# Kernel optimization log

Hardware: AMD Instinct MI355X
Metric: run time of the kernel (lower is better)

## Reference

```python
import jax, jax.numpy as jnp
import numpy as np
import math

B, T, E, H, DH, FH, L, V = 64, 256, 256, 8, 256, 1024, 6, 65
NEG = -1.0e9


def layer_norm(x, g, b, eps=1e-5):
    mu = jnp.mean(x, axis=-1, keepdims=True)
    var = jnp.var(x, axis=-1, keepdims=True)
    return (x - mu) / jnp.sqrt(var + eps) * g + b


def setup_inputs() -> dict:
    key = jax.random.key(0)
    ks = jax.random.split(key, 24)
    s = 0.02
    inp = {
        "tokens": jax.random.randint(ks[0], (B, T), 0, V, dtype=jnp.int32),
        "emb": jax.random.normal(ks[1], (V, E), jnp.float32) * s,
        # per-layer, per-head QKV weights stacked: [L, H, E, DH]
        "Wk": jax.random.normal(ks[2], (L, H, E, DH), jnp.float32) * s,
        "Wq": jax.random.normal(ks[3], (L, H, E, DH), jnp.float32) * s,
        "Wv": jax.random.normal(ks[4], (L, H, E, DH), jnp.float32) * s,
        "bk": jnp.zeros((L, H, DH), jnp.float32),
        "bq": jnp.zeros((L, H, DH), jnp.float32),
        "bv": jnp.zeros((L, H, DH), jnp.float32),
        "Wp": jax.random.normal(ks[5], (L, H * DH, E), jnp.float32) * s,
        "bp": jnp.zeros((L, E), jnp.float32),
        # one LayerNorm per block, reused twice (matches original module)
        "ln_g": jnp.ones((L, E), jnp.float32),
        "ln_b": jnp.zeros((L, E), jnp.float32),
        "W1": jax.random.normal(ks[6], (L, E, FH), jnp.float32) * s,
        "b1": jnp.zeros((L, FH), jnp.float32),
        "W2": jax.random.normal(ks[7], (L, FH, E), jnp.float32) * s,
        "b2": jnp.zeros((L, E), jnp.float32),
        "Wc1": jax.random.normal(ks[8], (E, FH), jnp.float32) * s,
        "bc1": jnp.zeros((FH,), jnp.float32),
        "Wc2": jax.random.normal(ks[9], (FH, V), jnp.float32) * s,
        "bc2": jnp.zeros((V,), jnp.float32),
    }
    return inp


def reference(tokens, emb, Wk, Wq, Wv, bk, bq, bv, Wp, bp, ln_g, ln_b,
              W1, b1, W2, b2, Wc1, bc1, Wc2, bc2):
    # embedding + (degenerate) positional encoding: pos table is all zeros,
    # so pos_encode reduces to x * sqrt(n_embd)
    x = emb[tokens] * math.sqrt(E)  # [B, T, E]
    # causal mask: positions where tril==0 (strict upper triangle) are masked
    mask = ~jnp.tril(jnp.ones((T, T), dtype=bool))  # True => masked
    scale = 1.0 / math.sqrt(DH)
    for i in range(L):
        K = jnp.einsum('bte,hed->bhtd', x, Wk[i]) + bk[i][None, :, None, :]
        Q = jnp.einsum('bte,hed->bhtd', x, Wq[i]) + bq[i][None, :, None, :]
        Vv = jnp.einsum('bte,hed->bhtd', x, Wv[i]) + bv[i][None, :, None, :]
        # NOTE: original computes Score = K @ Q^T (K and Q roles swapped)
        scores = jnp.einsum('bhtd,bhsd->bhts', K, Q) * scale
        scores = jnp.where(mask, NEG, scores)
        attn = jax.nn.softmax(scores, axis=-1)
        out = jnp.einsum('bhts,bhsd->bhtd', attn, Vv)  # [B,H,T,DH]
        out = out.transpose(0, 2, 1, 3).reshape(B, T, H * DH)
        proj = out @ Wp[i] + bp[i]
        mid = layer_norm(x + proj, ln_g[i], ln_b[i])
        ffn = jax.nn.relu(mid @ W1[i] + b1[i]) @ W2[i] + b2[i]
        x = layer_norm(mid + ffn, ln_g[i], ln_b[i])
    logits = jax.nn.relu(x @ Wc1 + bc1) @ Wc2 + bc2  # [B, T, V]
    return logits
```

## Files before the change

kernel.cpp:

```cpp
#include <hip/hip_runtime.h>
#include <hip/hip_bf16.h>

#define BB 64
#define TT 256
#define EE 256
#define HH 8
#define DHD 256
#define FFH 1024
#define LL 6
#define VV 65
#define NCHK 4
#define CB (BB / NCHK)
#define CNT (CB * TT)

typedef float f32x4 __attribute__((ext_vector_type(4)));
typedef short bf16x8 __attribute__((ext_vector_type(8)));
typedef unsigned short u16x8 __attribute__((ext_vector_type(8)));
typedef unsigned short u16x4 __attribute__((ext_vector_type(4)));

__device__ __forceinline__ unsigned short f2b(float f) {
  union { float f; unsigned u; } x; x.f = f;
  unsigned r = x.u + 0x7fffu + ((x.u >> 16) & 1u);
  return (unsigned short)(r >> 16);
}

#define BMT 128
#define BNT 128
#define BKT 32
#define LSTR 40

struct GP2 {
  const unsigned short* A; int lda; long sA;
  const unsigned short* B; int ldb; long sB;
  void* C; int ldc;
  int divC; long sC0, sC1;
  int rsplit; long sRowOuter;
  const float* bias; long sBias;
  const float* resid; int ldr;
  int N, K;
  float scale;
};

template<int OUTMODE, bool HAS_BIAS, bool RELU, bool HAS_RESID, bool MASKED,
         bool CAUSALK, bool NCHECK>
__global__ __launch_bounds__(256) void mfma_gemm(GP2 p) {
  __shared__ unsigned short As[BMT * LSTR];
  __shared__ unsigned short Bs[BNT * LSTR];
  const int tid  = threadIdx.x;
  const int m0   = blockIdx.x * BMT;
  const int n0   = blockIdx.y * BNT;
  const int z    = blockIdx.z;
  const int lane = tid & 63;
  const int wid  = tid >> 6;
  const int wm   = (wid >> 1) * 64, wn = (wid & 1) * 64;
  const int lr   = lane & 15;
  const int kq   = lane >> 4;

  const long zoff = (long)(z / p.divC) * p.sC0 + (long)(z % p.divC) * p.sC1;

  if constexpr (MASKED) {
    if (n0 >= m0 + BMT) {
      float* Cf = (float*)p.C;
#pragma unroll
      for (int fm = 0; fm < 4; ++fm)
#pragma unroll
        for (int r = 0; r < 4; ++r) {
          int m = m0 + wm + fm * 16 + kq * 4 + r;
          long ro = zoff + (long)(m / p.rsplit) * p.sRowOuter
                         + (long)(m % p.rsplit) * p.ldc;
#pragma unroll
          for (int fn = 0; fn < 4; ++fn) {
            int n = n0 + wn + fn * 16 + lr;
            Cf[ro + n] = -1.0e9f;
          }
        }
      return;
    }
  }

  const unsigned short* Az = p.A + (long)z * p.sA;
  const unsigned short* Bz = p.B + (long)z * p.sB;

  f32x4 acc[4][4] = {};

  const int kEnd = CAUSALK ? ((p.K < m0 + BMT) ? p.K : (m0 + BMT)) : p.K;
  for (int k0 = 0; k0 < kEnd; k0 += BKT) {
#pragma unroll
    for (int u0 = 0; u0 < 2; ++u0) {
      int u = tid + u0 * 256;
      int row = u >> 2, seg = (u & 3) << 3;
      u16x8 v = *(const u16x8*)(Az + (long)(m0 + row) * p.lda + (k0 + seg));
      *(u16x8*)&As[row * LSTR + seg] = v;
    }
#pragma unroll
    for (int u0 = 0; u0 < 2; ++u0) {
      int u = tid + u0 * 256;
      int row = u >> 2, seg = (u & 3) << 3;
      u16x8 v = {0, 0, 0, 0, 0, 0, 0, 0};
      if (!NCHECK || (n0 + row < p.N))
        v = *(const u16x8*)(Bz + (long)(n0 + row) * p.ldb + (k0 + seg));
      *(u16x8*)&Bs[row * LSTR + seg] = v;
    }
    __syncthreads();
    bf16x8 af[4], bv[4];
#pragma unroll
    for (int f = 0; f < 4; ++f) {
      af[f] = *(const bf16x8*)&As[(wm + f * 16 + lr) * LSTR + kq * 8];
      bv[f] = *(const bf16x8*)&Bs[(wn + f * 16 + lr) * LSTR + kq * 8];
    }
#pragma unroll
    for (int fm = 0; fm < 4; ++fm)
#pragma unroll
      for (int fn = 0; fn < 4; ++fn)
        acc[fm][fn] = __builtin_amdgcn_mfma_f32_16x16x32_bf16(
            af[fm], bv[fn], acc[fm][fn], 0, 0, 0);
    __syncthreads();
  }

  const float* bias = nullptr;
  if constexpr (HAS_BIAS) bias = p.bias + (long)z * p.sBias;

#pragma unroll
  for (int fm = 0; fm < 4; ++fm)
#pragma unroll
    for (int fn = 0; fn < 4; ++fn) {
      f32x4 a = acc[fm][fn];
      int n = n0 + wn + fn * 16 + lr;
      if constexpr (NCHECK) { if (n >= p.N) continue; }
      if constexpr (OUTMODE == 2) {
        int mb = m0 + wm + fm * 16 + kq * 4;
        long off = zoff + (long)(mb / p.rsplit) * p.sRowOuter
                        + (long)n * p.ldc + (mb % p.rsplit);
        u16x4 w;
#pragma unroll
        for (int r = 0; r < 4; ++r) {
          float v = a[r];
          if constexpr (HAS_BIAS) v += bias[n];
          w[r] = f2b(v);
        }
        *(u16x4*)((unsigned short*)p.C + off) = w;
      } else {
#pragma unroll
        for (int r = 0; r < 4; ++r) {
          int m = m0 + wm + fm * 16 + kq * 4 + r;
          long off = zoff + (long)(m / p.rsplit) * p.sRowOuter
                          + (long)(m % p.rsplit) * p.ldc + n;
          float v = a[r];
          if constexpr (HAS_BIAS) v += bias[n];
          if constexpr (MASKED) v = (n <= m) ? v * p.scale : -1.0e9f;
          if constexpr (HAS_RESID) v += p.resid[(long)m * p.ldr + n];
          if constexpr (RELU) v = fmaxf(v, 0.0f);
          if constexpr (OUTMODE == 0) ((float*)p.C)[off] = v;
          else ((unsigned short*)p.C)[off] = f2b(v);
        }
      }
    }
}

__global__ __launch_bounds__(256) void transpose_b_k(const float* __restrict__ in,
                                                     unsigned short* __restrict__ out,
                                                     int R, int C, long sIn, long sOut) {
  __shared__ float t[32][33];
  const int z = blockIdx.z;
  in += (long)z * sIn; out += (long)z * sOut;
  const int c0 = blockIdx.x * 32, r0 = blockIdx.y * 32;
  const int tx = threadIdx.x & 31, ty = threadIdx.x >> 5;
#pragma unroll
  for (int i = 0; i < 4; ++i) {
    int r = r0 + ty + i * 8;
    if (r < R && c0 + tx < C) t[ty + i * 8][tx] = in[(long)r * C + c0 + tx];
  }
  __syncthreads();
#pragma unroll
  for (int i = 0; i < 4; ++i) {
    int rr = r0 + tx, cc = c0 + ty + i * 8;
    if (rr < R && cc < C) out[(long)cc * R + rr] = f2b(t[tx][ty + i * 8]);
  }
}

__global__ __launch_bounds__(256) void softmax_k(const float* __restrict__ S,
                                                 unsigned short* __restrict__ P) {
  const int t = blockIdx.x;
  const long z = blockIdx.y;
  const float* row = S + z * (long)(TT * TT) + (long)t * TT;
  unsigned short* prow = P + z * (long)(TT * TT) + (long)t * TT;
  const int tid = threadIdx.x;
  float v = row[tid];
  float m = v;
#pragma unroll
  for (int off = 32; off; off >>= 1) m = fmaxf(m, __shfl_xor(m, off));
  __shared__ float red[8];
  if ((tid & 63) == 0) red[tid >> 6] = m;
  __syncthreads();
  m = fmaxf(fmaxf(red[0], red[1]), fmaxf(red[2], red[3]));
  float e = __expf(v - m);
  float s = e;
#pragma unroll
  for (int off = 32; off; off >>= 1) s += __shfl_xor(s, off);
  if ((tid & 63) == 0) red[4 + (tid >> 6)] = s;
  __syncthreads();
  s = red[4] + red[5] + red[6] + red[7];
  prow[tid] = f2b(e / s);
}

__global__ __launch_bounds__(256) void ln_k(float* __restrict__ x,
                                            unsigned short* __restrict__ xb,
                                            const float* __restrict__ g,
                                            const float* __restrict__ b) {
  const long row = blockIdx.x;
  const int tid = threadIdx.x;
  float* p = x + row * EE;
  float v = p[tid];
  float s = v, s2 = v * v;
#pragma unroll
  for (int off = 32; off; off >>= 1) {
    s += __shfl_xor(s, off);
    s2 += __shfl_xor(s2, off);
  }
  __shared__ float r1[4], r2[4];
  if ((tid & 63) == 0) { r1[tid >> 6] = s; r2[tid >> 6] = s2; }
  __syncthreads();
  s = r1[0] + r1[1] + r1[2] + r1[3];
  s2 = r2[0] + r2[1] + r2[2] + r2[3];
  float mu = s * (1.0f / EE);
  float var = fmaxf(s2 * (1.0f / EE) - mu * mu, 0.0f);
  float rn = rsqrtf(var + 1e-5f);
  float o = (v - mu) * rn * g[tid] + b[tid];
  p[tid] = o;
  xb[row * EE + tid] = f2b(o);
}

__global__ __launch_bounds__(256) void embed_k(const int* __restrict__ tok,
                                               const float* __restrict__ emb,
                                               float* __restrict__ X,
                                               unsigned short* __restrict__ Xb) {
  const long n = blockIdx.x;
  const int e = threadIdx.x;
  float v = emb[(long)tok[n] * EE + e] * 16.0f;
  X[n * EE + e] = v;
  Xb[n * EE + e] = f2b(v);
}

__global__ void tripwire_k(float* out, float code) { out[0] = code; }

extern "C" void kernel_launch(void* const* d_in, const int* in_sizes, int n_in,
                              void* d_out, int out_size, void* d_ws, size_t ws_size,
                              hipStream_t stream) {
  const int*   tokens = (const int*)d_in[0];
  const float* emb  = (const float*)d_in[1];
  const float* Wk   = (const float*)d_in[2];
  const float* Wq   = (const float*)d_in[3];
  const float* Wv   = (const float*)d_in[4];
  const float* bk   = (const float*)d_in[5];
  const float* bq   = (const float*)d_in[6];
  const float* bv   = (const float*)d_in[7];
  const float* Wp   = (const float*)d_in[8];
  const float* bp   = (const float*)d_in[9];
  const float* lng  = (const float*)d_in[10];
  const float* lnb  = (const float*)d_in[11];
  const float* W1   = (const float*)d_in[12];
  const float* b1   = (const float*)d_in[13];
  const float* W2   = (const float*)d_in[14];
  const float* b2   = (const float*)d_in[15];
  const float* Wc1  = (const float*)d_in[16];
  const float* bc1  = (const float*)d_in[17];
  const float* Wc2  = (const float*)d_in[18];
  const float* bc2  = (const float*)d_in[19];
  float* out = (float*)d_out;

  const long NT   = (long)BB * TT;
  const long CTD  = (long)CB * HH * TT * DHD;
  const long CTT  = (long)CB * HH * TT * TT;

  if (ws_size < 183109632UL) {
    tripwire_k<<<1, 1, 0, stream>>>(out, -100000.0f - (float)(ws_size >> 20));
    return;
  }

  char* w = (char*)d_ws;
  float* X   = (float*)w;            w += NT * EE * 4;
  float* MID = (float*)w;            w += NT * EE * 4;
  unsigned short* Xb   = (unsigned short*)w; w += NT * EE * 2;
  unsigned short* MIDb = (unsigned short*)w; w += NT * EE * 2;
  unsigned short* CK   = (unsigned short*)w; w += CTD * 2;
  unsigned short* CQ   = (unsigned short*)w; w += CTD * 2;
  unsigned short* CVt  = (unsigned short*)w; w += CTD * 2;
  float* CSb = (float*)w;            w += CTT * 4;
  unsigned short* CPb  = (unsigned short*)w; w += CTT * 2;
  unsigned short* Wkt  = (unsigned short*)w; w += (long)LL * HH * DHD * EE * 2;
  unsigned short* Wqt  = (unsigned short*)w; w += (long)LL * HH * DHD * EE * 2;
  unsigned short* Wvt  = (unsigned short*)w; w += (long)LL * HH * DHD * EE * 2;
  unsigned short* Wpt  = (unsigned short*)w; w += (long)LL * EE * (HH * DHD) * 2;
  unsigned short* W1t  = (unsigned short*)w; w += (long)LL * FFH * EE * 2;
  unsigned short* W2t  = (unsigned short*)w; w += (long)LL * EE * FFH * 2;
  unsigned short* Wc1t = (unsigned short*)w; w += (long)FFH * EE * 2;
  unsigned short* Wc2t = (unsigned short*)w; w += (long)VV * FFH * 2;
  unsigned short* AO = CK;
  unsigned short* H1 = (unsigned short*)CSb;

  transpose_b_k<<<dim3(8, 8, LL * HH), 256, 0, stream>>>(Wk, Wkt, EE, DHD, (long)EE * DHD, (long)DHD * EE);
  transpose_b_k<<<dim3(8, 8, LL * HH), 256, 0, stream>>>(Wq, Wqt, EE, DHD, (long)EE * DHD, (long)DHD * EE);
  transpose_b_k<<<dim3(8, 8, LL * HH), 256, 0, stream>>>(Wv, Wvt, EE, DHD, (long)EE * DHD, (long)DHD * EE);
  transpose_b_k<<<dim3(8, 64, LL), 256, 0, stream>>>(Wp, Wpt, HH * DHD, EE, (long)HH * DHD * EE, (long)EE * HH * DHD);
  transpose_b_k<<<dim3(32, 8, LL), 256, 0, stream>>>(W1, W1t, EE, FFH, (long)EE * FFH, (long)FFH * EE);
  transpose_b_k<<<dim3(8, 32, LL), 256, 0, stream>>>(W2, W2t, FFH, EE, (long)FFH * EE, (long)EE * FFH);
  transpose_b_k<<<dim3(32, 8, 1), 256, 0, stream>>>(Wc1, Wc1t, EE, FFH, 0, 0);
  transpose_b_k<<<dim3(3, 32, 1), 256, 0, stream>>>(Wc2, Wc2t, FFH, VV, 0, 0);

  embed_k<<<NT, 256, 0, stream>>>(tokens, emb, X, Xb);

  for (int i = 0; i < LL; ++i) {
    for (int c = 0; c < NCHK; ++c) {
      const long RB = (long)c * CNT;
      for (int m3 = 0; m3 < 3; ++m3) {
        GP2 p{};
        p.A = Xb + RB * EE; p.lda = EE; p.sA = 0;
        p.B = (m3 == 0 ? Wkt : m3 == 1 ? Wqt : Wvt) + (long)i * HH * DHD * EE;
        p.ldb = EE; p.sB = (long)DHD * EE;
        p.divC = 1; p.sC1 = 0;
        p.rsplit = TT;
        p.bias = (m3 == 0 ? bk : m3 == 1 ? bq : bv) + (long)i * HH * DHD;
        p.sBias = DHD;
        p.N = DHD; p.K = EE;
        if (m3 < 2) {
          p.C = (m3 == 0 ? CK : CQ); p.ldc = DHD;
          p.sC0 = (long)TT * DHD; p.sRowOuter = (long)HH * TT * DHD;
          mfma_gemm<1, true, false, false, false, false, false>
              <<<dim3(CNT / BMT, DHD / BNT, HH), 256, 0, stream>>>(p);
        } else {
          p.C = CVt; p.ldc = TT;
          p.sC0 = (long)DHD * TT; p.sRowOuter = (long)HH * DHD * TT;
          mfma_gemm<2, true, false, false, false, false, false>
              <<<dim3(CNT / BMT, DHD / BNT, HH), 256, 0, stream>>>(p);
        }
      }
      {
        GP2 p{};
        p.A = CK; p.lda = DHD; p.sA = (long)TT * DHD;
        p.B = CQ; p.ldb = DHD; p.sB = (long)TT * DHD;
        p.C = CSb; p.ldc = TT;
        p.divC = 1; p.sC0 = (long)TT * TT; p.sC1 = 0;
        p.rsplit = 1 << 30; p.sRowOuter = 0;
        p.N = TT; p.K = DHD; p.scale = 0.0625f;
        mfma_gemm<0, false, false, false, true, false, false>
            <<<dim3(TT / BMT, TT / BNT, CB * HH), 256, 0, stream>>>(p);
      }
      softmax_k<<<dim3(TT, CB * HH), 256, 0, stream>>>(CSb, CPb);
      {
        GP2 p{};
        p.A = CPb; p.lda = TT; p.sA = (long)TT * TT;
        p.B = CVt; p.ldb = TT; p.sB = (long)DHD * TT;
        p.C = AO; p.ldc = HH * DHD;
        p.divC = HH; p.sC0 = (long)TT * HH * DHD; p.sC1 = DHD;
        p.rsplit = 1 << 30; p.sRowOuter = 0;
        p.N = DHD; p.K = TT;
        mfma_gemm<1, false, false, false, false, true, false>
            <<<dim3(TT / BMT, DHD / BNT, CB * HH), 256, 0, stream>>>(p);
      }
      {
        GP2 p{};
        p.A = AO; p.lda = HH * DHD; p.sA = 0;
        p.B = Wpt + (long)i * EE * HH * DHD; p.ldb = HH * DHD; p.sB = 0;
        p.C = MID + RB * EE; p.ldc = EE;
        p.divC = 1; p.sC0 = 0; p.sC1 = 0; p.rsplit = 1 << 30; p.sRowOuter = 0;
        p.bias = bp + (long)i * EE; p.sBias = 0;
        p.resid = X + RB * EE; p.ldr = EE;
        p.N = EE; p.K = HH * DHD;
        mfma_gemm<0, true, false, true, false, false, false>
            <<<dim3(CNT / BMT, EE / BNT, 1), 256, 0, stream>>>(p);
      }
    }
    ln_k<<<NT, 256, 0, stream>>>(MID, MIDb, lng + (long)i * EE, lnb + (long)i * EE);
    {
      GP2 p{};
      p.A = MIDb; p.lda = EE; p.sA = 0;
      p.B = W1t + (long)i * FFH * EE; p.ldb = EE; p.sB = 0;
      p.C = H1; p.ldc = FFH;
      p.divC = 1; p.sC0 = 0; p.sC1 = 0; p.rsplit = 1 << 30; p.sRowOuter = 0;
      p.bias = b1 + (long)i * FFH; p.sBias = 0;
      p.N = FFH; p.K = EE;
      mfma_gemm<1, true, true, false, false, false, false>
          <<<dim3(NT / BMT, FFH / BNT, 1), 256, 0, stream>>>(p);
    }
    {
      GP2 p{};
      p.A = H1; p.lda = FFH; p.sA = 0;
      p.B = W2t + (long)i * EE * FFH; p.ldb = FFH; p.sB = 0;
      p.C = X; p.ldc = EE;
      p.divC = 1; p.sC0 = 0; p.sC1 = 0; p.rsplit = 1 << 30; p.sRowOuter = 0;
      p.bias = b2 + (long)i * EE; p.sBias = 0;
      p.resid = MID; p.ldr = EE;
      p.N = EE; p.K = FFH;
      mfma_gemm<0, true, false, true, false, false, false>
          <<<dim3(NT / BMT, EE / BNT, 1), 256, 0, stream>>>(p);
    }
    ln_k<<<NT, 256, 0, stream>>>(X, Xb, lng + (long)i * EE, lnb + (long)i * EE);
  }

  {
    GP2 p{};
    p.A = Xb; p.lda = EE; p.sA = 0;
    p.B = Wc1t; p.ldb = EE; p.sB = 0;
    p.C = H1; p.ldc = FFH;
    p.divC = 1; p.sC0 = 0; p.sC1 = 0; p.rsplit = 1 << 30; p.sRowOuter = 0;
    p.bias = bc1; p.sBias = 0;
    p.N = FFH; p.K = EE;
    mfma_gemm<1, true, true, false, false, false, false>
        <<<dim3(NT / BMT, FFH / BNT, 1), 256, 0, stream>>>(p);
  }
  {
    GP2 p{};
    p.A = H1; p.lda = FFH; p.sA = 0;
    p.B = Wc2t; p.ldb = FFH; p.sB = 0;
    p.C = out; p.ldc = VV;
    p.divC = 1; p.sC0 = 0; p.sC1 = 0; p.rsplit = 1 << 30; p.sRowOuter = 0;
    p.bias = bc2; p.sBias = 0;
    p.N = VV; p.K = FFH;
    mfma_gemm<0, true, false, false, false, false, true>
        <<<dim3(NT / BMT, 1, 1), 256, 0, stream>>>(p);
  }
}
```

Measured before the change: 4.695 ms.

## Fuse QKV projections into one GEMM, template tile sizes, adapt chunk count to workspace

Stacks the per-layer K, Q and V weights and biases so a single wide GEMM produces a packed KQV buffer per chunk, replacing three per-head launches. Attention GEMMs now read K, Q and V directly from the packed layout through new strides; PV loads V row-major and transposes it into shared memory. The GEMM kernel is templated on tile size, so the attention, output-projection, W2 and classifier GEMMs use 64x64 tiles to raise block count. The number of batch chunks is picked from the available workspace, so fewer, larger chunks run when memory allows. The scalar transposing shared-memory stores for V may cause bank conflicts, and the smaller tiles give less data reuse per block.

Result: faster. 3.871 ms (-17.6%).

```diff
diff --git a/kernel.cpp b/kernel.cpp
--- a/kernel.cpp
+++ b/kernel.cpp
@@ -6,17 +6,14 @@
 #define EE 256
 #define HH 8
 #define DHD 256
+#define HD2 2048
 #define FFH 1024
 #define LL 6
 #define VV 65
-#define NCHK 4
-#define CB (BB / NCHK)
-#define CNT (CB * TT)
 
 typedef float f32x4 __attribute__((ext_vector_type(4)));
 typedef short bf16x8 __attribute__((ext_vector_type(8)));
 typedef unsigned short u16x8 __attribute__((ext_vector_type(8)));
-typedef unsigned short u16x4 __attribute__((ext_vector_type(4)));
 
 __device__ __forceinline__ unsigned short f2b(float f) {
   union { float f; unsigned u; } x; x.f = f;
@@ -24,94 +21,102 @@
   return (unsigned short)(r >> 16);
 }
 
-#define BMT 128
-#define BNT 128
 #define BKT 32
 #define LSTR 40
 
-struct GP2 {
-  const unsigned short* A; int lda; long sA;
-  const unsigned short* B; int ldb; long sB;
-  void* C; int ldc;
-  int divC; long sC0, sC1;
-  int rsplit; long sRowOuter;
+struct GP3 {
+  const unsigned short* A; int lda; int divA; long sA0, sA1;
+  const unsigned short* B; int ldb; int divB; long sB0, sB1;
+  void* C; int ldc; int divC; long sC0, sC1;
   const float* bias; long sBias;
   const float* resid; int ldr;
   int N, K;
   float scale;
 };
 
-template<int OUTMODE, bool HAS_BIAS, bool RELU, bool HAS_RESID, bool MASKED,
-         bool CAUSALK, bool NCHECK>
-__global__ __launch_bounds__(256) void mfma_gemm(GP2 p) {
-  __shared__ unsigned short As[BMT * LSTR];
-  __shared__ unsigned short Bs[BNT * LSTR];
+template<int TM, int TN, int BSTAGE, int OUTMODE, bool HAS_BIAS, bool RELU,
+         bool HAS_RESID, bool MASKED, bool CAUSALK, bool NCH>
+__global__ __launch_bounds__(256) void gemmT(GP3 p) {
+  constexpr int FM = TM / 32, FN = TN / 32;
+  __shared__ unsigned short As[TM * LSTR];
+  __shared__ unsigned short Bs[TN * LSTR];
   const int tid  = threadIdx.x;
-  const int m0   = blockIdx.x * BMT;
-  const int n0   = blockIdx.y * BNT;
+  const int m0   = blockIdx.x * TM;
+  const int n0   = blockIdx.y * TN;
   const int z    = blockIdx.z;
   const int lane = tid & 63;
   const int wid  = tid >> 6;
-  const int wm   = (wid >> 1) * 64, wn = (wid & 1) * 64;
+  const int wm   = (wid >> 1) * (TM / 2), wn = (wid & 1) * (TN / 2);
   const int lr   = lane & 15;
   const int kq   = lane >> 4;
 
   const long zoff = (long)(z / p.divC) * p.sC0 + (long)(z % p.divC) * p.sC1;
 
   if constexpr (MASKED) {
-    if (n0 >= m0 + BMT) {
+    if (n0 >= m0 + TM) {
       float* Cf = (float*)p.C;
 #pragma unroll
-      for (int fm = 0; fm < 4; ++fm)
+      for (int fm = 0; fm < FM; ++fm)
 #pragma unroll
         for (int r = 0; r < 4; ++r) {
           int m = m0 + wm + fm * 16 + kq * 4 + r;
-          long ro = zoff + (long)(m / p.rsplit) * p.sRowOuter
-                         + (long)(m % p.rsplit) * p.ldc;
-#pragma unroll
-          for (int fn = 0; fn < 4; ++fn) {
+#pragma unroll
+          for (int fn = 0; fn < FN; ++fn) {
             int n = n0 + wn + fn * 16 + lr;
-            Cf[ro + n] = -1.0e9f;
+            Cf[zoff + (long)m * p.ldc + n] = -1.0e9f;
           }
         }
       return;
     }
   }
 
-  const unsigned short* Az = p.A + (long)z * p.sA;
-  const unsigned short* Bz = p.B + (long)z * p.sB;
-
-  f32x4 acc[4][4] = {};
-
-  const int kEnd = CAUSALK ? ((p.K < m0 + BMT) ? p.K : (m0 + BMT)) : p.K;
+  const unsigned short* Az = p.A + (long)(z / p.divA) * p.sA0 + (long)(z % p.divA) * p.sA1;
+  const unsigned short* Bz = p.B + (long)(z / p.divB) * p.sB0 + (long)(z % p.divB) * p.sB1;
+
+  f32x4 acc[FM][FN] = {};
+
+  const int kEnd = CAUSALK ? ((p.K < m0 + TM) ? p.K : (m0 + TM)) : p.K;
   for (int k0 = 0; k0 < kEnd; k0 += BKT) {
 #pragma unroll
-    for (int u0 = 0; u0 < 2; ++u0) {
+    for (int u0 = 0; u0 < TM / 64; ++u0) {
       int u = tid + u0 * 256;
       int row = u >> 2, seg = (u & 3) << 3;
       u16x8 v = *(const u16x8*)(Az + (long)(m0 + row) * p.lda + (k0 + seg));
       *(u16x8*)&As[row * LSTR + seg] = v;
     }
-#pragma unroll
-    for (int u0 = 0; u0 < 2; ++u0) {
-      int u = tid + u0 * 256;
-      int row = u >> 2, seg = (u & 3) << 3;
-      u16x8 v = {0, 0, 0, 0, 0, 0, 0, 0};
-      if (!NCHECK || (n0 + row < p.N))
-        v = *(const u16x8*)(Bz + (long)(n0 + row) * p.ldb + (k0 + seg));
-      *(u16x8*)&Bs[row * LSTR + seg] = v;
+    if constexpr (BSTAGE == 0) {
+#pragma unroll
+      for (int u0 = 0; u0 < TN / 64; ++u0) {
+        int u = tid + u0 * 256;
+        int row = u >> 2, seg = (u & 3) << 3;
+        u16x8 v = {0, 0, 0, 0, 0, 0, 0, 0};
+        if (!NCH || (n0 + row < p.N))
+          v = *(const u16x8*)(Bz + (long)(n0 + row) * p.ldb + (k0 + seg));
+        *(u16x8*)&Bs[row * LSTR + seg] = v;
+      }
+    } else {
+      constexpr int NOCT = TN / 8;
+#pragma unroll
+      for (int u0 = 0; u0 < TN / 64; ++u0) {
+        int idx = tid + u0 * 256;
+        int kk = idx / NOCT, n8 = (idx % NOCT) * 8;
+        u16x8 v = *(const u16x8*)(Bz + (long)(k0 + kk) * p.ldb + (n0 + n8));
+#pragma unroll
+        for (int j = 0; j < 8; ++j) Bs[(n8 + j) * LSTR + kk] = v[j];
+      }
     }
     __syncthreads();
-    bf16x8 af[4], bv[4];
-#pragma unroll
-    for (int f = 0; f < 4; ++f) {
+    bf16x8 af[FM], bv[FN];
+#pragma unroll
+    for (int f = 0; f < FM; ++f)
       af[f] = *(const bf16x8*)&As[(wm + f * 16 + lr) * LSTR + kq * 8];
+#pragma unroll
+    for (int f = 0; f < FN; ++f)
       bv[f] = *(const bf16x8*)&Bs[(wn + f * 16 + lr) * LSTR + kq * 8];
-    }
-#pragma unroll
-    for (int fm = 0; fm < 4; ++fm)
-#pragma unroll
-      for (int fn = 0; fn < 4; ++fn)
+#pragma unroll
+    for (int fm = 0; fm < FM; ++fm)
+#pragma unroll
+      for (int fn = 0; fn < FN; ++fn)
         acc[fm][fn] = __builtin_amdgcn_mfma_f32_16x16x32_bf16(
             af[fm], bv[fn], acc[fm][fn], 0, 0, 0);
     __syncthreads();
@@ -121,38 +126,23 @@
   if constexpr (HAS_BIAS) bias = p.bias + (long)z * p.sBias;
 
 #pragma unroll
-  for (int fm = 0; fm < 4; ++fm)
-#pragma unroll
-    for (int fn = 0; fn < 4; ++fn) {
+  for (int fm = 0; fm < FM; ++fm)
+#pragma unroll
+    for (int fn = 0; fn < FN; ++fn) {
       f32x4 a = acc[fm][fn];
       int n = n0 + wn + fn * 16 + lr;
-      if constexpr (NCHECK) { if (n >= p.N) continue; }
-      if constexpr (OUTMODE == 2) {
-        int mb = m0 + wm + fm * 16 + kq * 4;
-        long off = zoff + (long)(mb / p.rsplit) * p.sRowOuter
-                        + (long)n * p.ldc + (mb % p.rsplit);
-        u16x4 w;
-#pragma unroll
-        for (int r = 0; r < 4; ++r) {
-          float v = a[r];
-          if constexpr (HAS_BIAS) v += bias[n];
-          w[r] = f2b(v);
-        }
-        *(u16x4*)((unsigned short*)p.C + off) = w;
-      } else {
-#pragma unroll
-        for (int r = 0; r < 4; ++r) {
-          int m = m0 + wm + fm * 16 + kq * 4 + r;
-          long off = zoff + (long)(m / p.rsplit) * p.sRowOuter
-                          + (long)(m % p.rsplit) * p.ldc + n;
-          float v = a[r];
-          if constexpr (HAS_BIAS) v += bias[n];
-          if constexpr (MASKED) v = (n <= m) ? v * p.scale : -1.0e9f;
-          if constexpr (HAS_RESID) v += p.resid[(long)m * p.ldr + n];
-          if constexpr (RELU) v = fmaxf(v, 0.0f);
-          if constexpr (OUTMODE == 0) ((float*)p.C)[off] = v;
-          else ((unsigned short*)p.C)[off] = f2b(v);
-        }
+      if constexpr (NCH) { if (n >= p.N) continue; }
+#pragma unroll
+      for (int r = 0; r < 4; ++r) {
+        int m = m0 + wm + fm * 16 + kq * 4 + r;
+        long off = zoff + (long)m * p.ldc + n;
+        float v = a[r];
+        if constexpr (HAS_BIAS) v += bias[n];
+        if constexpr (MASKED) v = (n <= m) ? v * p.scale : -1.0e9f;
+        if constexpr (HAS_RESID) v += p.resid[(long)m * p.ldr + n];
+        if constexpr (RELU) v = fmaxf(v, 0.0f);
+        if constexpr (OUTMODE == 0) ((float*)p.C)[off] = v;
+        else ((unsigned short*)p.C)[off] = f2b(v);
       }
     }
 }
@@ -176,6 +166,18 @@
     int rr = r0 + tx, cc = c0 + ty + i * 8;
     if (rr < R && cc < C) out[(long)cc * R + rr] = f2b(t[tx][ty + i * 8]);
   }
+}
+
+__global__ __launch_bounds__(256) void stack_bias_k(const float* __restrict__ bk,
+                                                    const float* __restrict__ bq,
+                                                    const float* __restrict__ bv,
+                                                    float* __restrict__ dst) {
+  int idx = blockIdx.x * 256 + threadIdx.x;
+  int i = idx / (3 * HD2);
+  int r = idx % (3 * HD2);
+  int m3 = r / HD2, hd = r % HD2;
+  const float* s = (m3 == 0 ? bk : m3 == 1 ? bq : bv);
+  dst[idx] = s[(long)i * HD2 + hd];
 }
 
 __global__ __launch_bounds__(256) void softmax_k(const float* __restrict__ S,
@@ -268,40 +270,60 @@
   const float* bc2  = (const float*)d_in[19];
   float* out = (float*)d_out;
 
-  const long NT   = (long)BB * TT;
-  const long CTD  = (long)CB * HH * TT * DHD;
-  const long CTT  = (long)CB * HH * TT * TT;
-
-  if (ws_size < 183109632UL) {
+  const long NT = (long)BB * TT;
+
+  const size_t szX    = (size_t)NT * EE * 4;
+  const size_t szXb   = (size_t)NT * EE * 2;
+  const size_t szWqkv = (size_t)LL * 3 * HD2 * EE * 2;
+  const size_t szBqkv = (size_t)LL * 3 * HD2 * 4;
+  const size_t szWp   = (size_t)LL * EE * HD2 * 2;
+  const size_t szW1   = (size_t)LL * FFH * EE * 2;
+  const size_t szW2   = (size_t)LL * EE * FFH * 2;
+  const size_t szWc1  = (size_t)FFH * EE * 2;
+  const size_t szWc2  = (size_t)VV * FFH * 2;
+  const size_t fixed  = 2 * szX + 2 * szXb + szWqkv + szBqkv + szWp + szW1 + szW2 + szWc1 + szWc2;
+  const size_t chunkAll = (size_t)NT * 3 * HD2 * 2
+                        + (size_t)BB * HH * TT * TT * 4
+                        + (size_t)BB * HH * TT * TT * 2;
+
+  int nchk = 0;
+  for (int n : {1, 2, 4, 8})
+    if (ws_size >= fixed + chunkAll / n) { nchk = n; break; }
+  if (!nchk) {
     tripwire_k<<<1, 1, 0, stream>>>(out, -100000.0f - (float)(ws_size >> 20));
     return;
   }
+  const long CBr  = BB / nchk;
+  const long CNTr = NT / nchk;
 
   char* w = (char*)d_ws;
-  float* X   = (float*)w;            w += NT * EE * 4;
-  float* MID = (float*)w;            w += NT * EE * 4;
-  unsigned short* Xb   = (unsigned short*)w; w += NT * EE * 2;
-  unsigned short* MIDb = (unsigned short*)w; w += NT * EE * 2;
-  unsigned short* CK   = (unsigned short*)w; w += CTD * 2;
-  unsigned short* CQ   = (unsigned short*)w; w += CTD * 2;
-  unsigned short* CVt  = (unsigned short*)w; w += CTD * 2;
-  float* CSb = (float*)w;            w += CTT * 4;
-  unsigned short* CPb  = (unsigned short*)w; w += CTT * 2;
-  unsigned short* Wkt  = (unsigned short*)w; w += (long)LL * HH * DHD * EE * 2;
-  unsigned short* Wqt  = (unsigned short*)w; w += (long)LL * HH * DHD * EE * 2;
-  unsigned short* Wvt  = (unsigned short*)w; w += (long)LL * HH * DHD * EE * 2;
-  unsigned short* Wpt  = (unsigned short*)w; w += (long)LL * EE * (HH * DHD) * 2;
-  unsigned short* W1t  = (unsigned short*)w; w += (long)LL * FFH * EE * 2;
-  unsigned short* W2t  = (unsigned short*)w; w += (long)LL * EE * FFH * 2;
-  unsigned short* Wc1t = (unsigned short*)w; w += (long)FFH * EE * 2;
-  unsigned short* Wc2t = (unsigned short*)w; w += (long)VV * FFH * 2;
-  unsigned short* AO = CK;
-  unsigned short* H1 = (unsigned short*)CSb;
-
-  transpose_b_k<<<dim3(8, 8, LL * HH), 256, 0, stream>>>(Wk, Wkt, EE, DHD, (long)EE * DHD, (long)DHD * EE);
-  transpose_b_k<<<dim3(8, 8, LL * HH), 256, 0, stream>>>(Wq, Wqt, EE, DHD, (long)EE * DHD, (long)DHD * EE);
-  transpose_b_k<<<dim3(8, 8, LL * HH), 256, 0, stream>>>(Wv, Wvt, EE, DHD, (long)EE * DHD, (long)DHD * EE);
-  transpose_b_k<<<dim3(8, 64, LL), 256, 0, stream>>>(Wp, Wpt, HH * DHD, EE, (long)HH * DHD * EE, (long)EE * HH * DHD);
+  float* X   = (float*)w;  w += szX;
+  float* MID = (float*)w;  w += szX;
+  unsigned short* Xb   = (unsigned short*)w; w += szXb;
+  unsigned short* MIDb = (unsigned short*)w; w += szXb;
+  unsigned short* Wqkvt = (unsigned short*)w; w += szWqkv;
+  float*          bqkvs = (float*)w;          w += szBqkv;
+  unsigned short* Wpt  = (unsigned short*)w; w += szWp;
+  unsigned short* W1t  = (unsigned short*)w; w += szW1;
+  unsigned short* W2t  = (unsigned short*)w; w += szW2;
+  unsigned short* Wc1t = (unsigned short*)w; w += szWc1;
+  unsigned short* Wc2t = (unsigned short*)w; w += szWc2;
+  char* cbase = w;
+  unsigned short* KQV = (unsigned short*)cbase;
+  float* CS = (float*)(cbase + (size_t)CNTr * 3 * HD2 * 2);
+  unsigned short* CP = (unsigned short*)((char*)CS + (size_t)CBr * HH * TT * TT * 4);
+  unsigned short* AO = (unsigned short*)CS;
+  unsigned short* H1 = (unsigned short*)cbase;
+
+  for (int i = 0; i < LL; ++i)
+    for (int m3 = 0; m3 < 3; ++m3) {
+      const float* src = (m3 == 0 ? Wk : m3 == 1 ? Wq : Wv) + (long)i * HH * EE * DHD;
+      unsigned short* dst = Wqkvt + ((long)i * 3 * HD2 + m3 * HD2) * EE;
+      transpose_b_k<<<dim3(8, 8, HH), 256, 0, stream>>>(src, dst, EE, DHD,
+                                                        (long)EE * DHD, (long)DHD * EE);
+    }
+  stack_bias_k<<<(LL * 3 * HD2) / 256, 256, 0, stream>>>(bk, bq, bv, bqkvs);
+  transpose_b_k<<<dim3(8, 64, LL), 256, 0, stream>>>(Wp, Wpt, HD2, EE, (long)HD2 * EE, (long)EE * HD2);
   transpose_b_k<<<dim3(32, 8, LL), 256, 0, stream>>>(W1, W1t, EE, FFH, (long)EE * FFH, (long)FFH * EE);
   transpose_b_k<<<dim3(8, 32, LL), 256, 0, stream>>>(W2, W2t, FFH, EE, (long)FFH * EE, (long)EE * FFH);
   transpose_b_k<<<dim3(32, 8, 1), 256, 0, stream>>>(Wc1, Wc1t, EE, FFH, 0, 0);
@@ -310,113 +332,92 @@
   embed_k<<<NT, 256, 0, stream>>>(tokens, emb, X, Xb);
 
   for (int i = 0; i < LL; ++i) {
-    for (int c = 0; c < NCHK; ++c) {
-      const long RB = (long)c * CNT;
-      for (int m3 = 0; m3 < 3; ++m3) {
-        GP2 p{};
-        p.A = Xb + RB * EE; p.lda = EE; p.sA = 0;
-        p.B = (m3 == 0 ? Wkt : m3 == 1 ? Wqt : Wvt) + (long)i * HH * DHD * EE;
-        p.ldb = EE; p.sB = (long)DHD * EE;
-        p.divC = 1; p.sC1 = 0;
-        p.rsplit = TT;
-        p.bias = (m3 == 0 ? bk : m3 == 1 ? bq : bv) + (long)i * HH * DHD;
-        p.sBias = DHD;
-        p.N = DHD; p.K = EE;
-        if (m3 < 2) {
-          p.C = (m3 == 0 ? CK : CQ); p.ldc = DHD;
-          p.sC0 = (long)TT * DHD; p.sRowOuter = (long)HH * TT * DHD;
-          mfma_gemm<1, true, false, false, false, false, false>
-              <<<dim3(CNT / BMT, DHD / BNT, HH), 256, 0, stream>>>(p);
-        } else {
-          p.C = CVt; p.ldc = TT;
-          p.sC0 = (long)DHD * TT; p.sRowOuter = (long)HH * DHD * TT;
-          mfma_gemm<2, true, false, false, false, false, false>
-              <<<dim3(CNT / BMT, DHD / BNT, HH), 256, 0, stream>>>(p);
-        }
-      }
+    for (int c = 0; c < nchk; ++c) {
+      const long RB = (long)c * CNTr;
       {
-        GP2 p{};
-        p.A = CK; p.lda = DHD; p.sA = (long)TT * DHD;
-        p.B = CQ; p.ldb = DHD; p.sB = (long)TT * DHD;
-        p.C = CSb; p.ldc = TT;
-        p.divC = 1; p.sC0 = (long)TT * TT; p.sC1 = 0;
-        p.rsplit = 1 << 30; p.sRowOuter = 0;
+        GP3 p{};
+        p.A = Xb + RB * EE; p.lda = EE; p.divA = 1; p.sA0 = 0; p.sA1 = 0;
+        p.B = Wqkvt + (long)i * 3 * HD2 * EE; p.ldb = EE; p.divB = 1; p.sB0 = 0; p.sB1 = 0;
+        p.C = KQV; p.ldc = 3 * HD2; p.divC = 1; p.sC0 = 0; p.sC1 = 0;
+        p.bias = bqkvs + (long)i * 3 * HD2; p.sBias = 0;
+        p.N = 3 * HD2; p.K = EE;
+        gemmT<128, 128, 0, 1, true, false, false, false, false, false>
+            <<<dim3(CNTr / 128, (3 * HD2) / 128, 1), 256, 0, stream>>>(p);
+      }
+      {
+        GP3 p{};
+        p.A = KQV;        p.lda = 3 * HD2; p.divA = HH; p.sA0 = (long)TT * 3 * HD2; p.sA1 = DHD;
+        p.B = KQV + HD2;  p.ldb = 3 * HD2; p.divB = HH; p.sB0 = (long)TT * 3 * HD2; p.sB1 = DHD;
+        p.C = CS; p.ldc = TT; p.divC = 1; p.sC0 = (long)TT * TT; p.sC1 = 0;
         p.N = TT; p.K = DHD; p.scale = 0.0625f;
-        mfma_gemm<0, false, false, false, true, false, false>
-            <<<dim3(TT / BMT, TT / BNT, CB * HH), 256, 0, stream>>>(p);
-      }
-      softmax_k<<<dim3(TT, CB * HH), 256, 0, stream>>>(CSb, CPb);
+        gemmT<64, 64, 0, 0, false, false, false, true, false, false>
+            <<<dim3(4, 4, CBr * HH), 256, 0, stream>>>(p);
+      }
+      softmax_k<<<dim3(TT, CBr * HH), 256, 0, stream>>>(CS, CP);
       {
-        GP2 p{};
-        p.A = CPb; p.lda = TT; p.sA = (long)TT * TT;
-        p.B = CVt; p.ldb = TT; p.sB = (long)DHD * TT;
-        p.C = AO; p.ldc = HH * DHD;
-        p.divC = HH; p.sC0 = (long)TT * HH * DHD; p.sC1 = DHD;
-        p.rsplit = 1 << 30; p.sRowOuter = 0;
+        GP3 p{};
+        p.A = CP; p.lda = TT; p.divA = 1; p.sA0 = (long)TT * TT; p.sA1 = 0;
+        p.B = KQV + 2 * HD2; p.ldb = 3 * HD2; p.divB = HH; p.sB0 = (long)TT * 3 * HD2; p.sB1 = DHD;
+        p.C = AO; p.ldc = HD2; p.divC = HH; p.sC0 = (long)TT * HD2; p.sC1 = DHD;
         p.N = DHD; p.K = TT;
-        mfma_gemm<1, false, false, false, false, true, false>
-            <<<dim3(TT / BMT, DHD / BNT, CB * HH), 256, 0, stream>>>(p);
+        gemmT<64, 64, 1, 1, false, false, false, false, true, false>
+            <<<dim3(4, 4, CBr * HH), 256, 0, stream>>>(p);
       }
       {
-        GP2 p{};
-        p.A = AO; p.lda = HH * DHD; p.sA = 0;
-        p.B = Wpt + (long)i * EE * HH * DHD; p.ldb = HH * DHD; p.sB = 0;
-        p.C = MID + RB * EE; p.ldc = EE;
-        p.divC = 1; p.sC0 = 0; p.sC1 = 0; p.rsplit = 1 << 30; p.sRowOuter = 0;
+        GP3 p{};
+        p.A = AO; p.lda = HD2; p.divA = 1; p.sA0 = 0; p.sA1 = 0;
+        p.B = Wpt + (long)i * EE * HD2; p.ldb = HD2; p.divB = 1; p.sB0 = 0; p.sB1 = 0;
+        p.C = MID + RB * EE; p.ldc = EE; p.divC = 1; p.sC0 = 0; p.sC1 = 0;
         p.bias = bp + (long)i * EE; p.sBias = 0;
         p.resid = X + RB * EE; p.ldr = EE;
-        p.N = EE; p.K = HH * DHD;
-        mfma_gemm<0, true, false, true, false, false, false>
-            <<<dim3(CNT / BMT, EE / BNT, 1), 256, 0, stream>>>(p);
+        p.N = EE; p.K = HD2;
+        gemmT<64, 64, 0, 0, true, false, true, false, false, false>
+            <<<dim3(CNTr / 64, EE / 64, 1), 256, 0, stream>>>(p);
       }
     }
     ln_k<<<NT, 256, 0, stream>>>(MID, MIDb, lng + (long)i * EE, lnb + (long)i * EE);
     {
-      GP2 p{};
-      p.A = MIDb; p.lda = EE; p.sA = 0;
-      p.B = W1t + (long)i * FFH * EE; p.ldb = EE; p.sB = 0;
-      p.C = H1; p.ldc = FFH;
-      p.divC = 1; p.sC0 = 0; p.sC1 = 0; p.rsplit = 1 << 30; p.sRowOuter = 0;
+      GP3 p{};
+      p.A = MIDb; p.lda = EE; p.divA = 1; p.sA0 = 0; p.sA1 = 0;
+      p.B = W1t + (long)i * FFH * EE; p.ldb = EE; p.divB = 1; p.sB0 = 0; p.sB1 = 0;
+      p.C = H1; p.ldc = FFH; p.divC = 1; p.sC0 = 0; p.sC1 = 0;
       p.bias = b1 + (long)i * FFH; p.sBias = 0;
       p.N = FFH; p.K = EE;
-      mfma_gemm<1, true, true, false, false, false, false>
-          <<<dim3(NT / BMT, FFH / BNT, 1), 256, 0, stream>>>(p);
+      gemmT<128, 128, 0, 1, true, true, false, false, false, false>
+          <<<dim3(NT / 128, FFH / 128, 1), 256, 0, stream>>>(p);
     }
     {
-      GP2 p{};
-      p.A = H1; p.lda = FFH; p.sA = 0;
-      p.B = W2t + (long)i * EE * FFH; p.ldb = FFH; p.sB = 0;
-      p.C = X; p.ldc = EE;
-      p.divC = 1; p.sC0 = 0; p.sC1 = 0; p.rsplit = 1 << 30; p.sRowOuter = 0;
+      GP3 p{};
+      p.A = H1; p.lda = FFH; p.divA = 1; p.sA0 = 0; p.sA1 = 0;
+      p.B = W2t + (long)i * EE * FFH; p.ldb = FFH; p.divB = 1; p.sB0 = 0; p.sB1 = 0;
+      p.C = X; p.ldc = EE; p.divC = 1; p.sC0 = 0; p.sC1 = 0;
       p.bias = b2 + (long)i * EE; p.sBias = 0;
       p.resid = MID; p.ldr = EE;
       p.N = EE; p.K = FFH;
-      mfma_gemm<0, true, false, true, false, false, false>
-          <<<dim3(NT / BMT, EE / BNT, 1), 256, 0, stream>>>(p);
+      gemmT<64, 64, 0, 0, true, false, true, false, false, false>
+          <<<dim3(NT / 64, EE / 64, 1), 256, 0, stream>>>(p);
     }
     ln_k<<<NT, 256, 0, stream>>>(X, Xb, lng + (long)i * EE, lnb + (long)i * EE);
   }
 
   {
-    GP2 p{};
-    p.A = Xb; p.lda = EE; p.sA = 0;
-    p.B = Wc1t; p.ldb = EE; p.sB = 0;
-    p.C = H1; p.ldc = FFH;
-    p.divC = 1; p.sC0 = 0; p.sC1 = 0; p.rsplit = 1 << 30; p.sRowOuter = 0;
+    GP3 p{};
+    p.A = Xb; p.lda = EE; p.divA = 1; p.sA0 = 0; p.sA1 = 0;
+    p.B = Wc1t; p.ldb = EE; p.divB = 1; p.sB0 = 0; p.sB1 = 0;
+    p.C = H1; p.ldc = FFH; p.divC = 1; p.sC0 = 0; p.sC1 = 0;
     p.bias = bc1; p.sBias = 0;
     p.N = FFH; p.K = EE;
-    mfma_gemm<1, true, true, false, false, false, false>
-        <<<dim3(NT / BMT, FFH / BNT, 1), 256, 0, stream>>>(p);
+    gemmT<128, 128, 0, 1, true, true, false, false, false, false>
+        <<<dim3(NT / 128, FFH / 128, 1), 256, 0, stream>>>(p);
   }
   {
-    GP2 p{};
-    p.A = H1; p.lda = FFH; p.sA = 0;
-    p.B = Wc2t; p.ldb = FFH; p.sB = 0;
-    p.C = out; p.ldc = VV;
-    p.divC = 1; p.sC0 = 0; p.sC1 = 0; p.rsplit = 1 << 30; p.sRowOuter = 0;
+    GP3 p{};
+    p.A = H1; p.lda = FFH; p.divA = 1; p.sA0 = 0; p.sA1 = 0;
+    p.B = Wc2t; p.ldb = FFH; p.divB = 1; p.sB0 = 0; p.sB1 = 0;
+    p.C = out; p.ldc = VV; p.divC = 1; p.sC0 = 0; p.sC1 = 0;
     p.bias = bc2; p.sBias = 0;
     p.N = VV; p.K = FFH;
-    mfma_gemm<0, true, false, false, false, false, true>
-        <<<dim3(NT / BMT, 1, 1), 256, 0, stream>>>(p);
-  }
-}
+    gemmT<64, 64, 0, 0, true, false, false, false, false, true>
+        <<<dim3(NT / 64, 2, 1), 256, 0, stream>>>(p);
+  }
+}
```
